# Optimization experiments

Measured on AMD Instinct MI355X. Metric: run time of the kernel, lower is better.

The kernel has to match this reference:

```python
import jax, jax.numpy as jnp
import numpy as np

B, S, D = 2, 2048, 1024
H, HD, R = 16, 64, 128
BLOCK, TOPK = 64, 4
ROPE_BASE = 100000.0
NEG = -1e30  # finite large-negative instead of -inf to avoid NaN rows


def _rope_tables(seq_len, dim, dtype):
    inv_freq = 1.0 / (ROPE_BASE ** (jnp.arange(0, dim, 2, dtype=jnp.float32) / dim))
    freqs = jnp.arange(seq_len, dtype=jnp.float32)[:, None] * inv_freq[None, :]  # [S, dim/2]
    emb = jnp.concatenate([freqs, freqs], axis=-1)  # [S, dim]
    return jnp.cos(emb).astype(dtype), jnp.sin(emb).astype(dtype)


def _rotate_half(t):
    t1, t2 = jnp.split(t, 2, axis=-1)
    return jnp.concatenate([-t2, t1], axis=-1)


def _apply_rope(t, cos, sin):
    # t: [B, H, S, HD]; cos/sin: [S, HD]
    return t * cos[None, None] + _rotate_half(t) * sin[None, None]


def setup_inputs() -> dict:
    key = jax.random.key(0)
    ks = jax.random.split(key, 6)
    s = 0.02
    return {
        "x": jax.random.normal(ks[0], (B, S, D), jnp.float32),
        "w_q": jax.random.normal(ks[1], (D, D), jnp.float32) * s,
        "w_kv_down": jax.random.normal(ks[2], (R, D), jnp.float32) * s,
        "w_kv_up": jax.random.normal(ks[3], (2 * D, R), jnp.float32) * s,
        "w_out": jax.random.normal(ks[4], (D, D), jnp.float32) * s,
        "w_scorer": jax.random.normal(ks[5], (1, D), jnp.float32) * s,
    }


def reference(x, w_q, w_kv_down, w_kv_up, w_out, w_scorer):
    b, s, d = x.shape
    nb = s // BLOCK  # S divisible by block_size here

    q = (x @ w_q.T).reshape(b, s, H, HD).transpose(0, 2, 1, 3)  # [B,H,S,HD]
    latent = x @ w_kv_down.T                                      # [B,S,R]
    kv = latent @ w_kv_up.T                                       # [B,S,2D]
    k, v = jnp.split(kv, 2, axis=-1)
    k = k.reshape(b, s, H, HD).transpose(0, 2, 1, 3)
    v = v.reshape(b, s, H, HD).transpose(0, 2, 1, 3)

    cos, sin = _rope_tables(s, HD, x.dtype)
    q = _apply_rope(q, cos, sin)
    k = _apply_rope(k, cos, sin)

    # block relevance scores from mean-pooled block reps of x
    block_reps = x.reshape(b, nb, BLOCK, d).mean(axis=2)          # [B,nb,D]
    block_scores = (block_reps @ w_scorer.T)[..., 0]              # [B,nb]
    _, top_idx = jax.lax.top_k(block_scores, min(TOPK, nb))       # [B,topk]

    # sparse key mask: True where key position lies in a selected block
    sel = jnp.zeros((b, nb), dtype=bool)
    sel = sel.at[jnp.arange(b)[:, None], top_idx].set(True)       # [B,nb]
    sparse_mask = jnp.repeat(sel, BLOCK, axis=1)                  # [B,S]

    causal = jnp.tril(jnp.ones((s, s), dtype=bool))               # True = allowed
    allowed = sparse_mask[:, None, None, :] & causal[None, None]  # [B,1,S,S]

    scale = 1.0 / jnp.sqrt(jnp.asarray(HD, x.dtype))
    scores = jnp.einsum("bhqd,bhkd->bhqk", q, k) * scale          # [B,H,S,S]
    scores = jnp.where(allowed, scores, NEG)
    attn = jax.nn.softmax(scores, axis=-1)
    out = jnp.einsum("bhqk,bhkd->bhqd", attn, v)                  # [B,H,S,HD]
    out = out.transpose(0, 2, 1, 3).reshape(b, s, d)
    return out @ w_out.T
```

## Files before the change

kernel.cpp:

```cpp
#include <hip/hip_runtime.h>
#include <hip/hip_bf16.h>
#include <math.h>

#define B_ 2
#define S_ 2048
#define D_ 1024
#define H_ 16
#define HD_ 64
#define R_ 128
#define NBLK 32
#define TOPK_ 4
#define BS_ (B_*S_)

typedef __attribute__((ext_vector_type(8))) short bf16x8;
typedef __attribute__((ext_vector_type(4))) float f32x4;

__device__ __forceinline__ unsigned short f2bf(float f) {
    unsigned int u = __float_as_uint(f);
    u += 0x7fffu + ((u >> 16) & 1u);
    return (unsigned short)(u >> 16);
}
__device__ __forceinline__ float bf2f(unsigned short h) {
    return __uint_as_float(((unsigned int)h) << 16);
}
__device__ __forceinline__ unsigned int pack2(float a, float b) {
    return (unsigned int)f2bf(a) | ((unsigned int)f2bf(b) << 16);
}
__device__ __forceinline__ void gload_lds16(const void* g, void* l) {
    __builtin_amdgcn_global_load_lds((const __attribute__((address_space(1))) void*)g,
                                     (__attribute__((address_space(3))) void*)l, 16, 0, 0);
}

__global__ void rope_tables_k(float* __restrict__ cosT, float* __restrict__ sinT) {
    int idx = blockIdx.x*256 + threadIdx.x;
    if (idx >= S_*HD_) return;
    int s  = idx >> 6;
    int hd = idx & 63;
    int j = (hd < 32) ? hd : hd - 32;
    float inv = powf(100000.0f, -((float)(2*j) / 64.0f));
    float fr = (float)s * inv;
    cosT[idx] = cosf(fr);
    sinT[idx] = sinf(fr);
}

__global__ __launch_bounds__(256) void cvtw_k(const float* __restrict__ wq,
        const float* __restrict__ wkd, const float* __restrict__ wku,
        const float* __restrict__ wo, unsigned short* __restrict__ wcat,
        unsigned short* __restrict__ wkub, unsigned short* __restrict__ wob) {
    const int blk = blockIdx.x;
    const float* src; unsigned short* dst; int base;
    if      (blk < 512) { src = wq;  dst = wcat;            base = blk;       }
    else if (blk < 576) { src = wkd; dst = wcat + 1048576;  base = blk - 512; }
    else if (blk < 704) { src = wku; dst = wkub;            base = blk - 576; }
    else                { src = wo;  dst = wob;             base = blk - 704; }
    const int i = base*2048 + threadIdx.x*8;
    float4 a = *(const float4*)&src[i];
    float4 b = *(const float4*)&src[i+4];
    uint4 o;
    o.x = pack2(a.x, a.y); o.y = pack2(a.z, a.w);
    o.z = pack2(b.x, b.y); o.w = pack2(b.z, b.w);
    *(uint4*)&dst[i] = o;
}

template<int EPI>
__global__ __launch_bounds__(256) void gemm_mfma_k(const unsigned short* __restrict__ A,
        const unsigned short* __restrict__ Bm, int M, int N, int K,
        void* __restrict__ o0, void* __restrict__ o1,
        const float* __restrict__ cosT, const float* __restrict__ sinT,
        float* __restrict__ vsum) {
    __shared__ unsigned short shbuf[2][12288];
    const int tid  = threadIdx.x;
    const int wave = tid >> 6, lane = tid & 63;
    const int nx = N >> 6;
    const int ob = blockIdx.x;
    const int w  = ((ob & 7) * (gridDim.x >> 3)) + (ob >> 3);
    const int bm = (w / nx) << 7, bn = (w % nx) << 6;
    const int g  = lane >> 4, qc = lane & 15;
    const int srow  = lane >> 3;
    const int sslot = (lane & 7) ^ srow;

    f32x4 acc[2][4];
    #pragma unroll
    for (int m=0;m<2;m++)
        #pragma unroll
        for (int n=0;n<4;n++)
            acc[m][n] = (f32x4){0.f,0.f,0.f,0.f};

    const int NT = K >> 6;
    auto STAGE = [&](int buf, int t) {
        const int k0 = t << 6;
        unsigned short* As = shbuf[buf];
        unsigned short* Bs = shbuf[buf] + 8192;
        #pragma unroll
        for (int it = 0; it < 4; ++it) {
            const int chunk = (it << 2) | wave;
            const int row   = (chunk << 3) | srow;
            gload_lds16(A + (size_t)(bm + row) * K + k0 + (sslot << 3), &As[chunk << 9]);
        }
        #pragma unroll
        for (int it = 0; it < 2; ++it) {
            const int chunk = (it << 2) | wave;
            const int row   = (chunk << 3) | srow;
            gload_lds16(Bm + (size_t)(bn + row) * K + k0 + (sslot << 3), &Bs[chunk << 9]);
        }
    };

    STAGE(0, 0);
    __syncthreads();
    for (int t = 0; t < NT; ++t) {
        if (t + 1 < NT) STAGE((t + 1) & 1, t + 1);
        const unsigned short* As = shbuf[t & 1];
        const unsigned short* Bs = shbuf[t & 1] + 8192;
        #pragma unroll
        for (int ks = 0; ks < 2; ++ks) {
            const int swb = ((ks << 2) | g) ^ (lane & 7);
            bf16x8 af[2], bfr[4];
            #pragma unroll
            for (int m = 0; m < 2; ++m)
                af[m]  = *(const bf16x8*)&As[(((wave << 5) + (m << 4) + qc) << 6) + (swb << 3)];
            #pragma unroll
            for (int n = 0; n < 4; ++n)
                bfr[n] = *(const bf16x8*)&Bs[(((n << 4) + qc) << 6) + (swb << 3)];
            #pragma unroll
            for (int m = 0; m < 2; ++m)
                #pragma unroll
                for (int n = 0; n < 4; ++n)
                    acc[m][n] = __builtin_amdgcn_mfma_f32_16x16x32_bf16(af[m], bfr[n], acc[m][n], 0, 0, 0);
        }
        __syncthreads();
    }

    if (EPI == 0) {
        float* C = (float*)o0;
        #pragma unroll
        for (int m = 0; m < 2; ++m) {
            const int r0 = bm + (wave << 5) + (m << 4) + (g << 2);
            #pragma unroll
            for (int n = 0; n < 4; ++n) {
                const int c = bn + (n << 4) + qc;
                #pragma unroll
                for (int j = 0; j < 4; ++j)
                    C[(size_t)(r0 + j) * N + c] = acc[m][n][j];
            }
        }
    } else {
        const bool isrope = (bn < 1024);
        if (isrope) {
            const int h = bn >> 6;
            unsigned short* dst = (unsigned short*)o0;
            #pragma unroll
            for (int m = 0; m < 2; ++m) {
                const int r0 = bm + (wave << 5) + (m << 4) + (g << 2);
                #pragma unroll
                for (int j = 0; j < 4; ++j) {
                    const int row = r0 + j;
                    const int b = row >> 11, s = row & (S_-1);
                    const size_t obase = ((size_t)(b*H_ + h) * S_ + s) << 6;
                    #pragma unroll
                    for (int n = 0; n < 4; ++n) {
                        const int hd = (n << 4) + qc;
                        const float c_ = cosT[(s << 6) + hd];
                        const float sn = sinT[(s << 6) + hd];
                        const float rot = (n < 2) ? -acc[m][n ^ 2][j] : acc[m][n ^ 2][j];
                        dst[obase + hd] = f2bf(acc[m][n][j] * c_ + rot * sn);
                    }
                }
            }
        } else if (EPI == 1) {
            unsigned short* latb = (unsigned short*)o1;
            const int c0 = bn - 1024;
            #pragma unroll
            for (int m = 0; m < 2; ++m) {
                const int r0 = bm + (wave << 5) + (m << 4) + (g << 2);
                #pragma unroll
                for (int n = 0; n < 4; ++n) {
                    const int c = c0 + (n << 4) + qc;
                    #pragma unroll
                    for (int j = 0; j < 4; ++j)
                        latb[(size_t)(r0 + j) * R_ + c] = f2bf(acc[m][n][j]);
                }
            }
        } else {
            const int h  = (bn >> 6) - 16;
            const int b  = bm >> 11, s0 = bm & (S_-1);
            const int bh = (b << 4) + h;
            unsigned short* vtb = (unsigned short*)o1;
            unsigned short (*T)[72] = (unsigned short(*)[72])&shbuf[0][0];
            #pragma unroll
            for (int m = 0; m < 2; ++m) {
                const int r0 = (wave << 5) + (m << 4) + (g << 2);
                #pragma unroll
                for (int n = 0; n < 4; ++n)
                    #pragma unroll
                    for (int j = 0; j < 4; ++j)
                        T[r0 + j][(n << 4) + qc] = f2bf(acc[m][n][j]);
            }
            __syncthreads();
            #pragma unroll
            for (int u = 0; u < 2; ++u) {
                const int kb = (s0 >> 6) + u;
                unsigned short* dst = vtb + (((size_t)(bh * NBLK + kb)) << 12);
                #pragma unroll
                for (int uu = 0; uu < 2; ++uu) {
                    const int idx = (uu << 8) + tid;
                    const int dd = idx >> 3, k0 = (idx & 7) << 3;
                    unsigned short tmp[8];
                    float sm = 0.f;
                    #pragma unroll
                    for (int j = 0; j < 8; ++j) { tmp[j] = T[(u << 6) + k0 + j][dd]; sm += bf2f(tmp[j]); }
                    *(uint4*)&dst[(size_t)(dd << 6) + k0] = *(uint4*)tmp;
                    sm += __shfl_xor(sm, 1);
                    sm += __shfl_xor(sm, 2);
                    sm += __shfl_xor(sm, 4);
                    if ((tid & 7) == 0) atomicAdd(&vsum[(bh << 6) + dd], sm);
                }
            }
        }
    }
}

__global__ __launch_bounds__(256) void rowscore_cvt_k(const float* __restrict__ x,
        const float* __restrict__ wsc, float* __restrict__ rows,
        unsigned short* __restrict__ xb) {
    const int wid  = (blockIdx.x << 2) + (threadIdx.x >> 6);
    const int lane = threadIdx.x & 63;
    #pragma unroll
    for (int r = 0; r < 4; ++r) {
        const int row = (wid << 2) + r;
        const float* xp = x + (size_t)row * D_;
        unsigned short* xo = xb + (size_t)row * D_;
        float acc = 0.f;
        #pragma unroll
        for (int j = 0; j < 4; ++j) {
            const int off = ((j << 6) + lane) << 2;
            float4 xv = *(const float4*)&xp[off];
            float4 wv = *(const float4*)&wsc[off];
            acc = fmaf(xv.x, wv.x, acc);
            acc = fmaf(xv.y, wv.y, acc);
            acc = fmaf(xv.z, wv.z, acc);
            acc = fmaf(xv.w, wv.w, acc);
            uint2 o; o.x = pack2(xv.x, xv.y); o.y = pack2(xv.z, xv.w);
            *(uint2*)&xo[off] = o;
        }
        #pragma unroll
        for (int m = 1; m <= 32; m <<= 1) acc += __shfl_xor(acc, m);
        if (lane == 0) rows[row] = acc;
    }
}

__global__ __launch_bounds__(256) void blocktopk_k(const float* __restrict__ rows,
        int* __restrict__ sel) {
    __shared__ float bs[64];
    const int bk = threadIdx.x >> 2, qt = threadIdx.x & 3;
    const float* rp = rows + (bk << 6) + (qt << 4);
    float p = 0.f;
    #pragma unroll
    for (int i = 0; i < 16; ++i) p += rp[i];
    p += __shfl_xor(p, 1);
    p += __shfl_xor(p, 2);
    if (qt == 0) bs[bk] = p;
    __syncthreads();
    if (threadIdx.x < B_) {
        const int b = threadIdx.x;
        float sc[NBLK];
        for (int i = 0; i < NBLK; ++i) sc[i] = bs[b * NBLK + i];
        for (int j = 0; j < TOPK_; ++j) {
            float best = -INFINITY; int bi = 0;
            for (int i = 0; i < NBLK; ++i)
                if (sc[i] > best) { best = sc[i]; bi = i; }
            sel[b * TOPK_ + j] = bi;
            sc[bi] = -INFINITY;
        }
    }
}

__global__ __launch_bounds__(256) void attn_mfma_k(const unsigned short* __restrict__ qrb,
        const unsigned short* __restrict__ krb, const unsigned short* __restrict__ vtb,
        const int* __restrict__ sel, const float* __restrict__ vsum,
        unsigned short* __restrict__ attno) {
    const int qb = blockIdx.x & (NBLK-1);
    const int bh = blockIdx.x >> 5;
    const int b  = bh >> 4;
    const int h  = bh & 15;
    const int tid  = threadIdx.x;
    const int wave = tid >> 6, lane = tid & 63;
    const int g = lane >> 4, qc = lane & 15;

    __shared__ unsigned short Ks[64][72];
    __shared__ unsigned short Vt[64][72];
    __shared__ unsigned short Pl[4][16][72];
    __shared__ float cfl[4][16];
    __shared__ float lvl[4][16];

    int selb[4];
    #pragma unroll
    for (int j=0;j<4;j++) selb[j] = sel[(b<<2)+j];
    const bool diag = (selb[0]==qb)|(selb[1]==qb)|(selb[2]==qb)|(selb[3]==qb);

    const unsigned short* qp = qrb + (((size_t)bh*S_ + (qb<<6) + (wave<<4) + qc) << 6);
    bf16x8 bq[2];
    bq[0] = *(const bf16x8*)(qp + (g<<3));
    bq[1] = *(const bf16x8*)(qp + 32 + (g<<3));

    f32x4 oacc[4];
    #pragma unroll
    for (int n=0;n<4;n++) oacc[n] = (f32x4){0.f,0.f,0.f,0.f};
    float mrun = -INFINITY, lrun = 0.f;
    int nproc = 0;
    const int qib = (wave<<4) + qc;

    for (int j = 0; j < 5; ++j) {
        int kb; bool isdiag;
        if (j < 4) { kb = selb[j]; isdiag = false; if (kb >= qb) continue; }
        else       { if (!diag) continue; kb = qb; isdiag = true; }
        nproc++;
        const uint4* gk = (const uint4*)(krb + (((size_t)bh*S_ + (kb<<6)) << 6));
        const uint4* gv = (const uint4*)(vtb + (((size_t)(bh*NBLK + kb)) << 12));
        __syncthreads();
        #pragma unroll
        for (int u=0;u<2;u++) {
            int idx = (u<<8) + tid;
            int r = idx>>3, c = (idx&7)<<3;
            *(uint4*)&Ks[r][c] = gk[idx];
            *(uint4*)&Vt[r][c] = gv[idx];
        }
        __syncthreads();

        f32x4 sf[4];
        #pragma unroll
        for (int m=0;m<4;m++) sf[m] = (f32x4){0.f,0.f,0.f,0.f};
        #pragma unroll
        for (int ks=0;ks<2;ks++)
            #pragma unroll
            for (int m=0;m<4;m++) {
                bf16x8 ak = *(const bf16x8*)&Ks[(m<<4)+qc][(ks<<5)+(g<<3)];
                sf[m] = __builtin_amdgcn_mfma_f32_16x16x32_bf16(ak, bq[ks], sf[m], 0, 0, 0);
            }

        float s[16];
        float bmax = -INFINITY;
        #pragma unroll
        for (int m=0;m<4;m++)
            #pragma unroll
            for (int r2=0;r2<4;r2++) {
                const int kl = (m<<4)+(g<<2)+r2;
                float v = sf[m][r2]*0.125f;
                if (isdiag && kl > qib) v = -1e30f;
                s[(m<<2)+r2] = v;
                bmax = fmaxf(bmax, v);
            }
        bmax = fmaxf(bmax, __shfl_xor(bmax, 16));
        bmax = fmaxf(bmax, __shfl_xor(bmax, 32));
        const float mnew = fmaxf(mrun, bmax);
        const float cf = __expf(mrun - mnew);
        float ls = 0.f;
        #pragma unroll
        for (int m=0;m<4;m++) {
            float p0 = __expf(s[(m<<2)+0]-mnew);
            float p1 = __expf(s[(m<<2)+1]-mnew);
            float p2 = __expf(s[(m<<2)+2]-mnew);
            float p3 = __expf(s[(m<<2)+3]-mnew);
            ls += p0+p1+p2+p3;
            const int koff = (m<<4)+(g<<2);
            *(unsigned int*)&Pl[wave][qc][koff]   = pack2(p0,p1);
            *(unsigned int*)&Pl[wave][qc][koff+2] = pack2(p2,p3);
        }
        ls += __shfl_xor(ls, 16);
        ls += __shfl_xor(ls, 32);
        lrun = lrun*cf + ls;
        cfl[wave][qc] = cf;
        f32x4 cf4 = *(const f32x4*)&cfl[wave][g<<2];
        #pragma unroll
        for (int n=0;n<4;n++) oacc[n] *= cf4;
        #pragma unroll
        for (int ks=0;ks<2;ks++) {
            bf16x8 pa = *(const bf16x8*)&Pl[wave][qc][(ks<<5)+(g<<3)];
            #pragma unroll
            for (int n=0;n<4;n++) {
                bf16x8 vb = *(const bf16x8*)&Vt[(n<<4)+qc][(ks<<5)+(g<<3)];
                oacc[n] = __builtin_amdgcn_mfma_f32_16x16x32_bf16(pa, vb, oacc[n], 0, 0, 0);
            }
        }
        mrun = mnew;
    }

    f32x4 il4 = (f32x4){0.f,0.f,0.f,0.f};
    if (nproc) {
        lvl[wave][qc] = 1.0f / lrun;
        il4 = *(const f32x4*)&lvl[wave][g<<2];
    }
    #pragma unroll
    for (int n=0;n<4;n++)
        #pragma unroll
        for (int r2=0;r2<4;r2++) {
            float val = nproc ? oacc[n][r2]*il4[r2]
                              : vsum[(bh<<6)+(n<<4)+qc] * (1.0f/(float)S_);
            const int row = (qb<<6) + (wave<<4) + (g<<2) + r2;
            attno[(((size_t)(b*S_+row))<<10) + (h<<6) + (n<<4) + qc] = f2bf(val);
        }
}

extern "C" void kernel_launch(void* const* d_in, const int* in_sizes, int n_in,
                              void* d_out, int out_size, void* d_ws, size_t ws_size,
                              hipStream_t stream) {
    (void)in_sizes; (void)n_in; (void)out_size; (void)ws_size;
    const float* x     = (const float*)d_in[0];
    const float* w_q   = (const float*)d_in[1];
    const float* w_kvd = (const float*)d_in[2];
    const float* w_kvu = (const float*)d_in[3];
    const float* w_o   = (const float*)d_in[4];
    const float* w_sc  = (const float*)d_in[5];
    float* out = (float*)d_out;

    char* p = (char*)d_ws;
    auto alloc = [&](size_t bytes) -> void* {
        void* r = (void*)p;
        p += (bytes + 255) & ~(size_t)255;
        return r;
    };
    float* cosT  = (float*)alloc((size_t)S_*HD_*4);
    float* sinT  = (float*)alloc((size_t)S_*HD_*4);
    unsigned short* xb    = (unsigned short*)alloc((size_t)BS_*D_*2);
    unsigned short* wcat  = (unsigned short*)alloc((size_t)(D_+R_)*D_*2);
    unsigned short* wkub  = (unsigned short*)alloc((size_t)2*D_*R_*2);
    unsigned short* wob   = (unsigned short*)alloc((size_t)D_*D_*2);
    unsigned short* latb  = (unsigned short*)alloc((size_t)BS_*R_*2);
    unsigned short* qrb   = (unsigned short*)alloc((size_t)BS_*D_*2);
    unsigned short* krb   = (unsigned short*)alloc((size_t)BS_*D_*2);
    unsigned short* vtb   = (unsigned short*)alloc((size_t)BS_*D_*2);
    unsigned short* attnob= (unsigned short*)alloc((size_t)BS_*D_*2);
    float* rows   = (float*)alloc((size_t)BS_*4);
    int*   sel    = (int*)  alloc((size_t)B_*TOPK_*4);
    float* vsum   = (float*)alloc((size_t)B_*H_*HD_*4);

    rope_tables_k<<<(S_*HD_+255)/256, 256, 0, stream>>>(cosT, sinT);
    cvtw_k<<<1216, 256, 0, stream>>>(w_q, w_kvd, w_kvu, w_o, wcat, wkub, wob);
    rowscore_cvt_k<<<256, 256, 0, stream>>>(x, w_sc, rows, xb);
    blocktopk_k<<<1, 256, 0, stream>>>(rows, sel);

    gemm_mfma_k<1><<<576, 256, 0, stream>>>(
        xb, wcat, BS_, D_+R_, D_, qrb, latb, cosT, sinT, nullptr);
    hipMemsetAsync(vsum, 0, (size_t)B_*H_*HD_*4, stream);
    gemm_mfma_k<2><<<1024, 256, 0, stream>>>(
        latb, wkub, BS_, 2*D_, R_, krb, vtb, cosT, sinT, vsum);

    attn_mfma_k<<<B_*H_*NBLK, 256, 0, stream>>>(qrb, krb, vtb, sel, vsum, attnob);
    gemm_mfma_k<0><<<512, 256, 0, stream>>>(
        attnob, wob, BS_, D_, D_, out, nullptr, nullptr, nullptr, nullptr);
}
```

Baseline: 152.6 us.

## Merge prep kernels, fold vsum memset into topk, async swizzled LDS loads in attention

Merges the rope table, weight conversion and row-score/x conversion kernels into one launch, and moves the vsum zeroing from a memset into the top-k kernel. This removes per-launch overhead for several small kernels and one memset. The attention kernel now builds a compact list of key blocks ahead of the loop. It loads K/V tiles with global_load_lds into unpadded, XOR-swizzled shared memory instead of staging them through registers into padded arrays. The aim is lower LDS staging cost and fewer bank conflicts, at the cost of more complex indexing.

Measured after the change: 143.0 us. -6.3%, faster.

```diff
diff --git a/kernel.cpp b/kernel.cpp
--- a/kernel.cpp
+++ b/kernel.cpp
@@ -31,35 +31,91 @@
                                      (__attribute__((address_space(3))) void*)l, 16, 0, 0);
 }
 
-__global__ void rope_tables_k(float* __restrict__ cosT, float* __restrict__ sinT) {
-    int idx = blockIdx.x*256 + threadIdx.x;
-    if (idx >= S_*HD_) return;
-    int s  = idx >> 6;
-    int hd = idx & 63;
-    int j = (hd < 32) ? hd : hd - 32;
-    float inv = powf(100000.0f, -((float)(2*j) / 64.0f));
-    float fr = (float)s * inv;
-    cosT[idx] = cosf(fr);
-    sinT[idx] = sinf(fr);
-}
-
-__global__ __launch_bounds__(256) void cvtw_k(const float* __restrict__ wq,
+__global__ __launch_bounds__(256) void prep_k(const float* __restrict__ x,
+        const float* __restrict__ wsc, const float* __restrict__ wq,
         const float* __restrict__ wkd, const float* __restrict__ wku,
-        const float* __restrict__ wo, unsigned short* __restrict__ wcat,
-        unsigned short* __restrict__ wkub, unsigned short* __restrict__ wob) {
+        const float* __restrict__ wo, float* __restrict__ cosT,
+        float* __restrict__ sinT, unsigned short* __restrict__ wcat,
+        unsigned short* __restrict__ wkub, unsigned short* __restrict__ wob,
+        float* __restrict__ rows, unsigned short* __restrict__ xb) {
     const int blk = blockIdx.x;
-    const float* src; unsigned short* dst; int base;
-    if      (blk < 512) { src = wq;  dst = wcat;            base = blk;       }
-    else if (blk < 576) { src = wkd; dst = wcat + 1048576;  base = blk - 512; }
-    else if (blk < 704) { src = wku; dst = wkub;            base = blk - 576; }
-    else                { src = wo;  dst = wob;             base = blk - 704; }
-    const int i = base*2048 + threadIdx.x*8;
-    float4 a = *(const float4*)&src[i];
-    float4 b = *(const float4*)&src[i+4];
-    uint4 o;
-    o.x = pack2(a.x, a.y); o.y = pack2(a.z, a.w);
-    o.z = pack2(b.x, b.y); o.w = pack2(b.z, b.w);
-    *(uint4*)&dst[i] = o;
+    if (blk < 512) {
+        const int idx = blk*256 + threadIdx.x;
+        const int s  = idx >> 6;
+        const int hd = idx & 63;
+        const int j = (hd < 32) ? hd : hd - 32;
+        const float inv = powf(100000.0f, -((float)(2*j) / 64.0f));
+        const float fr = (float)s * inv;
+        cosT[idx] = cosf(fr);
+        sinT[idx] = sinf(fr);
+    } else if (blk < 1728) {
+        const int wb = blk - 512;
+        const float* src; unsigned short* dst; int base;
+        if      (wb < 512) { src = wq;  dst = wcat;            base = wb;       }
+        else if (wb < 576) { src = wkd; dst = wcat + 1048576;  base = wb - 512; }
+        else if (wb < 704) { src = wku; dst = wkub;            base = wb - 576; }
+        else               { src = wo;  dst = wob;             base = wb - 704; }
+        const int i = base*2048 + threadIdx.x*8;
+        float4 a = *(const float4*)&src[i];
+        float4 b = *(const float4*)&src[i+4];
+        uint4 o;
+        o.x = pack2(a.x, a.y); o.y = pack2(a.z, a.w);
+        o.z = pack2(b.x, b.y); o.w = pack2(b.z, b.w);
+        *(uint4*)&dst[i] = o;
+    } else {
+        const int wid  = ((blk - 1728) << 2) + (threadIdx.x >> 6);
+        const int lane = threadIdx.x & 63;
+        #pragma unroll
+        for (int r = 0; r < 4; ++r) {
+            const int row = (wid << 2) + r;
+            const float* xp = x + (size_t)row * D_;
+            unsigned short* xo = xb + (size_t)row * D_;
+            float acc = 0.f;
+            #pragma unroll
+            for (int j = 0; j < 4; ++j) {
+                const int off = ((j << 6) + lane) << 2;
+                float4 xv = *(const float4*)&xp[off];
+                float4 wv = *(const float4*)&wsc[off];
+                acc = fmaf(xv.x, wv.x, acc);
+                acc = fmaf(xv.y, wv.y, acc);
+                acc = fmaf(xv.z, wv.z, acc);
+                acc = fmaf(xv.w, wv.w, acc);
+                uint2 o; o.x = pack2(xv.x, xv.y); o.y = pack2(xv.z, xv.w);
+                *(uint2*)&xo[off] = o;
+            }
+            #pragma unroll
+            for (int m = 1; m <= 32; m <<= 1) acc += __shfl_xor(acc, m);
+            if (lane == 0) rows[row] = acc;
+        }
+    }
+}
+
+__global__ __launch_bounds__(256) void blocktopk_k(const float* __restrict__ rows,
+        int* __restrict__ sel, float* __restrict__ vsum) {
+    ((float4*)vsum)[threadIdx.x]       = (float4){0.f,0.f,0.f,0.f};
+    ((float4*)vsum)[threadIdx.x + 256] = (float4){0.f,0.f,0.f,0.f};
+    __shared__ float bs[64];
+    const int bk = threadIdx.x >> 2, qt = threadIdx.x & 3;
+    const float* rp = rows + (bk << 6) + (qt << 4);
+    float p = 0.f;
+    #pragma unroll
+    for (int i = 0; i < 16; ++i) p += rp[i];
+    p += __shfl_xor(p, 1);
+    p += __shfl_xor(p, 2);
+    if (qt == 0) bs[bk] = p;
+    __syncthreads();
+    if (threadIdx.x < B_) {
+        const int b = threadIdx.x;
+        float sc[NBLK];
+        for (int i = 0; i < NBLK; ++i) sc[i] = bs[b * NBLK + i];
+        for (int j = 0; j < TOPK_; ++j) {
+            float best = -INFINITY; int bi = 0;
+            for (int i = 0; i < NBLK; ++i)
+                if (sc[i] > best) { best = sc[i]; bi = i; }
+            sel[b * TOPK_ + j] = bi;
+            sc[bi] = -INFINITY;
+        }
+    }
 }
 
 template<int EPI>
@@ -219,61 +275,6 @@
     }
 }
 
-__global__ __launch_bounds__(256) void rowscore_cvt_k(const float* __restrict__ x,
-        const float* __restrict__ wsc, float* __restrict__ rows,
-        unsigned short* __restrict__ xb) {
-    const int wid  = (blockIdx.x << 2) + (threadIdx.x >> 6);
-    const int lane = threadIdx.x & 63;
-    #pragma unroll
-    for (int r = 0; r < 4; ++r) {
-        const int row = (wid << 2) + r;
-        const float* xp = x + (size_t)row * D_;
-        unsigned short* xo = xb + (size_t)row * D_;
-        float acc = 0.f;
-        #pragma unroll
-        for (int j = 0; j < 4; ++j) {
-            const int off = ((j << 6) + lane) << 2;
-            float4 xv = *(const float4*)&xp[off];
-            float4 wv = *(const float4*)&wsc[off];
-            acc = fmaf(xv.x, wv.x, acc);
-            acc = fmaf(xv.y, wv.y, acc);
-            acc = fmaf(xv.z, wv.z, acc);
-            acc = fmaf(xv.w, wv.w, acc);
-            uint2 o; o.x = pack2(xv.x, xv.y); o.y = pack2(xv.z, xv.w);
-            *(uint2*)&xo[off] = o;
-        }
-        #pragma unroll
-        for (int m = 1; m <= 32; m <<= 1) acc += __shfl_xor(acc, m);
-        if (lane == 0) rows[row] = acc;
-    }
-}
-
-__global__ __launch_bounds__(256) void blocktopk_k(const float* __restrict__ rows,
-        int* __restrict__ sel) {
-    __shared__ float bs[64];
-    const int bk = threadIdx.x >> 2, qt = threadIdx.x & 3;
-    const float* rp = rows + (bk << 6) + (qt << 4);
-    float p = 0.f;
-    #pragma unroll
-    for (int i = 0; i < 16; ++i) p += rp[i];
-    p += __shfl_xor(p, 1);
-    p += __shfl_xor(p, 2);
-    if (qt == 0) bs[bk] = p;
-    __syncthreads();
-    if (threadIdx.x < B_) {
-        const int b = threadIdx.x;
-        float sc[NBLK];
-        for (int i = 0; i < NBLK; ++i) sc[i] = bs[b * NBLK + i];
-        for (int j = 0; j < TOPK_; ++j) {
-            float best = -INFINITY; int bi = 0;
-            for (int i = 0; i < NBLK; ++i)
-                if (sc[i] > best) { best = sc[i]; bi = i; }
-            sel[b * TOPK_ + j] = bi;
-            sc[bi] = -INFINITY;
-        }
-    }
-}
-
 __global__ __launch_bounds__(256) void attn_mfma_k(const unsigned short* __restrict__ qrb,
         const unsigned short* __restrict__ krb, const unsigned short* __restrict__ vtb,
         const int* __restrict__ sel, const float* __restrict__ vsum,
@@ -286,8 +287,8 @@
     const int wave = tid >> 6, lane = tid & 63;
     const int g = lane >> 4, qc = lane & 15;
 
-    __shared__ unsigned short Ks[64][72];
-    __shared__ unsigned short Vt[64][72];
+    __shared__ unsigned short Ks[64*64];
+    __shared__ unsigned short Vt[64*64];
     __shared__ unsigned short Pl[4][16][72];
     __shared__ float cfl[4][16];
     __shared__ float lvl[4][16];
@@ -296,6 +297,12 @@
     #pragma unroll
     for (int j=0;j<4;j++) selb[j] = sel[(b<<2)+j];
     const bool diag = (selb[0]==qb)|(selb[1]==qb)|(selb[2]==qb)|(selb[3]==qb);
+
+    int kbl[5]; int cnt = 0;
+    #pragma unroll
+    for (int j=0;j<4;j++) if (selb[j] < qb) kbl[cnt++] = selb[j];
+    const int dstart = cnt;
+    if (diag) kbl[cnt++] = qb;
 
     const unsigned short* qp = qrb + (((size_t)bh*S_ + (qb<<6) + (wave<<4) + qc) << 6);
     bf16x8 bq[2];
@@ -306,23 +313,23 @@
     #pragma unroll
     for (int n=0;n<4;n++) oacc[n] = (f32x4){0.f,0.f,0.f,0.f};
     float mrun = -INFINITY, lrun = 0.f;
-    int nproc = 0;
     const int qib = (wave<<4) + qc;
 
-    for (int j = 0; j < 5; ++j) {
-        int kb; bool isdiag;
-        if (j < 4) { kb = selb[j]; isdiag = false; if (kb >= qb) continue; }
-        else       { if (!diag) continue; kb = qb; isdiag = true; }
-        nproc++;
-        const uint4* gk = (const uint4*)(krb + (((size_t)bh*S_ + (kb<<6)) << 6));
-        const uint4* gv = (const uint4*)(vtb + (((size_t)(bh*NBLK + kb)) << 12));
+    const int srow = lane >> 3;
+    const int sslot = (lane & 7) ^ srow;
+
+    for (int i = 0; i < cnt; ++i) {
+        const int kb = kbl[i];
+        const bool isdiag = (i >= dstart);
+        const unsigned short* kB = krb + (((size_t)bh*S_ + (kb<<6)) << 6);
+        const unsigned short* vT = vtb + (((size_t)(bh*NBLK + kb)) << 12);
         __syncthreads();
         #pragma unroll
-        for (int u=0;u<2;u++) {
-            int idx = (u<<8) + tid;
-            int r = idx>>3, c = (idx&7)<<3;
-            *(uint4*)&Ks[r][c] = gk[idx];
-            *(uint4*)&Vt[r][c] = gv[idx];
+        for (int it = 0; it < 2; ++it) {
+            const int chunk = (it << 2) | wave;
+            const int row = (chunk << 3) | srow;
+            gload_lds16(kB + (row << 6) + (sslot << 3), &Ks[chunk << 9]);
+            gload_lds16(vT + (row << 6) + (sslot << 3), &Vt[chunk << 9]);
         }
         __syncthreads();
 
@@ -333,7 +340,8 @@
         for (int ks=0;ks<2;ks++)
             #pragma unroll
             for (int m=0;m<4;m++) {
-                bf16x8 ak = *(const bf16x8*)&Ks[(m<<4)+qc][(ks<<5)+(g<<3)];
+                const int sw = (((ks<<2)|g) ^ (qc & 7)) << 3;
+                bf16x8 ak = *(const bf16x8*)&Ks[(((m<<4)+qc)<<6) + sw];
                 sf[m] = __builtin_amdgcn_mfma_f32_16x16x32_bf16(ak, bq[ks], sf[m], 0, 0, 0);
             }
 
@@ -377,7 +385,8 @@
             bf16x8 pa = *(const bf16x8*)&Pl[wave][qc][(ks<<5)+(g<<3)];
             #pragma unroll
             for (int n=0;n<4;n++) {
-                bf16x8 vb = *(const bf16x8*)&Vt[(n<<4)+qc][(ks<<5)+(g<<3)];
+                const int sw = (((ks<<2)|g) ^ (qc & 7)) << 3;
+                bf16x8 vb = *(const bf16x8*)&Vt[(((n<<4)+qc)<<6) + sw];
                 oacc[n] = __builtin_amdgcn_mfma_f32_16x16x32_bf16(pa, vb, oacc[n], 0, 0, 0);
             }
         }
@@ -385,7 +394,7 @@
     }
 
     f32x4 il4 = (f32x4){0.f,0.f,0.f,0.f};
-    if (nproc) {
+    if (cnt) {
         lvl[wave][qc] = 1.0f / lrun;
         il4 = *(const f32x4*)&lvl[wave][g<<2];
     }
@@ -393,8 +402,8 @@
     for (int n=0;n<4;n++)
         #pragma unroll
         for (int r2=0;r2<4;r2++) {
-            float val = nproc ? oacc[n][r2]*il4[r2]
-                              : vsum[(bh<<6)+(n<<4)+qc] * (1.0f/(float)S_);
+            float val = cnt ? oacc[n][r2]*il4[r2]
+                            : vsum[(bh<<6)+(n<<4)+qc] * (1.0f/(float)S_);
             const int row = (qb<<6) + (wave<<4) + (g<<2) + r2;
             attno[(((size_t)(b*S_+row))<<10) + (h<<6) + (n<<4) + qc] = f2bf(val);
         }
@@ -433,14 +442,12 @@
     int*   sel    = (int*)  alloc((size_t)B_*TOPK_*4);
     float* vsum   = (float*)alloc((size_t)B_*H_*HD_*4);
 
-    rope_tables_k<<<(S_*HD_+255)/256, 256, 0, stream>>>(cosT, sinT);
-    cvtw_k<<<1216, 256, 0, stream>>>(w_q, w_kvd, w_kvu, w_o, wcat, wkub, wob);
-    rowscore_cvt_k<<<256, 256, 0, stream>>>(x, w_sc, rows, xb);
-    blocktopk_k<<<1, 256, 0, stream>>>(rows, sel);
+    prep_k<<<1984, 256, 0, stream>>>(x, w_sc, w_q, w_kvd, w_kvu, w_o,
+                                     cosT, sinT, wcat, wkub, wob, rows, xb);
+    blocktopk_k<<<1, 256, 0, stream>>>(rows, sel, vsum);
 
     gemm_mfma_k<1><<<576, 256, 0, stream>>>(
         xb, wcat, BS_, D_+R_, D_, qrb, latb, cosT, sinT, nullptr);
-    hipMemsetAsync(vsum, 0, (size_t)B_*H_*HD_*4, stream);
     gemm_mfma_k<2><<<1024, 256, 0, stream>>>(
         latb, wkub, BS_, 2*D_, R_, krb, vtb, cosT, sinT, vsum);
 
```
